# Kernel optimization log

Hardware: AMD Instinct MI355X
Metric: run time of the kernel (lower is better)

## Reference

```python
import jax, jax.numpy as jnp
import numpy as np

QMIN, QMAX = -128.0, 127.0  # int8 range


def setup_inputs() -> dict:
    key = jax.random.key(0)
    k1, k2, k3, k4 = jax.random.split(key, 4)
    B, S, K, O = 8, 2048, 4096, 4096
    x = jax.random.normal(k1, (B, S, K), dtype=jnp.float32)
    weight = jax.random.normal(k2, (O, K), dtype=jnp.float32)
    bias = jax.random.normal(k3, (O,), dtype=jnp.float32)
    # per-tensor activation qparams (static, from calibration observer)
    act_scale = jnp.ones((1,), dtype=jnp.float32) * 0.05
    act_zp = jnp.zeros((1,), dtype=jnp.int32)
    # per-output-row weight qparams (block_size = (1, in_features))
    weight_scale = jax.random.uniform(k4, (O, 1), dtype=jnp.float32,
                                      minval=0.005, maxval=0.02)
    weight_zp = jnp.zeros((O, 1), dtype=jnp.int32)
    return {"x": x, "weight": weight, "bias": bias,
            "act_scale": act_scale, "weight_scale": weight_scale,
            "act_zp": act_zp, "weight_zp": weight_zp}


def _quant_dequant(v, scale, zp):
    # affine quantize to int8 grid, then dequantize (simulated int8 math)
    q = jnp.clip(jnp.round(v / scale) + zp.astype(v.dtype), QMIN, QMAX)
    return (q - zp.astype(v.dtype)) * scale


def reference(x, weight, bias, act_scale, weight_scale, act_zp, weight_zp):
    # static per-tensor activation quantization
    dqx = _quant_dequant(x, act_scale, act_zp)          # [B, S, K]
    # per-row weight quantization
    dqw = _quant_dequant(weight, weight_scale, weight_zp)  # [O, K]
    # F.linear: x @ W^T + b
    return jnp.einsum('bsk,ok->bso', dqx, dqw) + bias
```

## Files before the change

kernel.cpp:

```cpp
#include <hip/hip_runtime.h>
#include <cstdint>
#include <cstddef>

typedef __attribute__((ext_vector_type(4)))  int   i32x4;
typedef __attribute__((ext_vector_type(16))) int   i32x16;
typedef __attribute__((ext_vector_type(4)))  float f32x4;

#define M_DIM 16384
#define N_DIM 4096
#define K_DIM 4096
#define NT    (K_DIM / 128)

#define BARRIER() asm volatile("s_barrier" ::: "memory")

__global__ __launch_bounds__(256) void quant_x_kernel(
    const float* __restrict__ x,
    const float* __restrict__ act_scale,
    const int*   __restrict__ act_zp,
    signed char* __restrict__ xq)
{
    int idx = blockIdx.x * 256 + threadIdx.x;
    float s   = act_scale[0];
    float zpf = (float)act_zp[0];
    const f32x4* xp = (const f32x4*)(x + (size_t)idx * 16);
    union { signed char c[16]; i32x4 v; } u;
#pragma unroll
    for (int j = 0; j < 4; ++j) {
        f32x4 v = xp[j];
#pragma unroll
        for (int e = 0; e < 4; ++e) {
            float q = rintf(v[e] / s) + zpf;
            q = fminf(fmaxf(q, -128.f), 127.f);
            u.c[j * 4 + e] = (signed char)(int)(q - zpf);
        }
    }
    *(i32x4*)(xq + (size_t)idx * 16) = u.v;
}

__global__ __launch_bounds__(256) void quant_w_kernel(
    const float* __restrict__ w,
    const float* __restrict__ wscale,
    const int*   __restrict__ wzp,
    signed char* __restrict__ wq)
{
    int idx = blockIdx.x * 256 + threadIdx.x;
    int row = idx >> 8;
    float s   = wscale[row];
    float zpf = (float)wzp[row];
    const f32x4* wp = (const f32x4*)(w + (size_t)idx * 16);
    union { signed char c[16]; i32x4 v; } u;
#pragma unroll
    for (int j = 0; j < 4; ++j) {
        f32x4 v = wp[j];
#pragma unroll
        for (int e = 0; e < 4; ++e) {
            float q = rintf(v[e] / s) + zpf;
            q = fminf(fmaxf(q, -128.f), 127.f);
            u.c[j * 4 + e] = (signed char)(int)(q - zpf);
        }
    }
    *(i32x4*)(wq + (size_t)idx * 16) = u.v;
}

__global__ __launch_bounds__(512, 2) void gemm_i8_256(
    const signed char* __restrict__ Aq,
    const signed char* __restrict__ Bq,
    const float* __restrict__ bias,
    const float* __restrict__ act_scale,
    const float* __restrict__ wscale,
    float* __restrict__ out)
{
    __shared__ signed char lds[65536];

    const int nbn = N_DIM / 256;
    const int nwg = (M_DIM / 256) * nbn;
    int bid = blockIdx.x;
    int wg  = (bid & 7) * (nwg >> 3) + (bid >> 3);
    int bm  = wg / nbn;
    int bn  = wg % nbn;

    int tid  = threadIdx.x;
    int wave = tid >> 6;
    int lane = tid & 63;
    int wm_i = wave >> 2;
    int wn_i = wave & 3;

    const signed char* Ag = Aq + (size_t)bm * 256 * K_DIM;
    const signed char* Bg = Bq + (size_t)bn * 256 * K_DIM;

    size_t soff = (size_t)(tid >> 1) * K_DIM + (((tid & 1) ^ ((tid >> 3) & 1)) * 16);

    int xbit  = (((lane >> 5) ^ ((lane >> 2) & 1)) << 4);
    int abase = wm_i * 4096 + (lane & 31) * 32 + xbit;
    int bbase = 32768 + wn_i * 2048 + (lane & 31) * 32 + xbit;

#define STAGE_AB(tile, s) do {                                                       \
    __builtin_amdgcn_global_load_lds(                                                \
        (const __attribute__((address_space(1))) void*)                              \
            (Ag + (size_t)(tile) * 128 + (s) * 32 + soff),                           \
        (__attribute__((address_space(3))) void*)(lds + (s) * 8192 + wave * 1024),   \
        16, 0, 0);                                                                   \
    __builtin_amdgcn_global_load_lds(                                                \
        (const __attribute__((address_space(1))) void*)                              \
            (Bg + (size_t)(tile) * 128 + (s) * 32 + soff),                           \
        (__attribute__((address_space(3))) void*)(lds + 32768 + (s) * 8192           \
                                                  + wave * 1024),                    \
        16, 0, 0);                                                                   \
} while (0)

#define READ_SET(AF, BF, s) do {                                                     \
    _Pragma("unroll")                                                                \
    for (int mf = 0; mf < 4; ++mf)                                                   \
        AF[mf] = *(const i32x4*)(lds + (s) * 8192 + abase + mf * 1024);              \
    _Pragma("unroll")                                                                \
    for (int nf = 0; nf < 2; ++nf)                                                   \
        BF[nf] = *(const i32x4*)(lds + (s) * 8192 + bbase + nf * 1024);              \
} while (0)

#define MFMA_SET(AF, BF) do {                                                        \
    _Pragma("unroll")                                                                \
    for (int mf = 0; mf < 4; ++mf)                                                   \
        _Pragma("unroll")                                                            \
        for (int nf = 0; nf < 2; ++nf)                                               \
            acc[mf][nf] = __builtin_amdgcn_mfma_i32_32x32x32_i8(                     \
                AF[mf], BF[nf], acc[mf][nf], 0, 0, 0);                               \
} while (0)

    i32x16 acc[4][2] = {};
    i32x4 aE[4], bE[2], aO[4], bO[2];

    STAGE_AB(0, 0); STAGE_AB(0, 1); STAGE_AB(0, 2); STAGE_AB(0, 3);
    asm volatile("s_waitcnt vmcnt(0)" ::: "memory");
    BARRIER();
    READ_SET(aE, bE, 0);
    asm volatile("s_waitcnt lgkmcnt(0)" ::: "memory");
    BARRIER();

#define PHASE(t, s, CA, CB, NA, NB) do {                                             \
    if ((t) + 1 < NT) {                                                              \
        STAGE_AB((t) + 1, (s));                                                      \
        if ((s) == 3) READ_SET(NA, NB, 0);               \
    }                                                                                \
    if ((s) < 3) READ_SET(NA, NB, (s) + 1);                         \
    __builtin_amdgcn_s_setprio(1);                                                   \
    MFMA_SET(CA, CB);                                                                \
    __builtin_amdgcn_s_setprio(0);                                                   \
    asm volatile("s_waitcnt lgkmcnt(0)" ::: "memory");                               \
    if ((t) < NT - 1) {                                                              \
        asm volatile("s_waitcnt vmcnt(4)" ::: "memory");                             \
    } else if ((s) == 0) {                                                           \
        asm volatile("s_waitcnt vmcnt(2)" ::: "memory");                             \
    } else if ((s) == 1) {                                                           \
        asm volatile("s_waitcnt vmcnt(0)" ::: "memory");                             \
    }                                                                                \
    BARRIER();                                                                       \
} while (0)

    for (int t = 0; t < NT; ++t) {
        PHASE(t, 0, aE, bE, aO, bO);
        PHASE(t, 1, aO, bO, aE, bE);
        PHASE(t, 2, aE, bE, aO, bO);
        PHASE(t, 3, aO, bO, aE, bE);
    }
#undef PHASE
#undef MFMA_SET
#undef READ_SET
#undef STAGE_AB

    float sa = act_scale[0];
#pragma unroll
    for (int nf = 0; nf < 2; ++nf) {
        int o = bn * 256 + wn_i * 64 + nf * 32 + (lane & 31);
        float sw = sa * wscale[o];
        float bv = bias[o];
#pragma unroll
        for (int mf = 0; mf < 4; ++mf) {
            int rowb = bm * 256 + wm_i * 128 + mf * 32 + 4 * (lane >> 5);
#pragma unroll
            for (int r = 0; r < 16; ++r) {
                int grow = rowb + (r & 3) + 8 * (r >> 2);
                out[(size_t)grow * N_DIM + o] = (float)acc[mf][nf][r] * sw + bv;
            }
        }
    }
}

__global__ void fallback_kernel(
    const float* __restrict__ x, const float* __restrict__ w,
    const float* __restrict__ bias,
    const float* __restrict__ act_scale, const float* __restrict__ wscale,
    const int* __restrict__ act_zp, const int* __restrict__ wzp,
    float* __restrict__ out)
{
    size_t idx = (size_t)blockIdx.x * blockDim.x + threadIdx.x;
    if (idx >= (size_t)M_DIM * N_DIM) return;
    int m = (int)(idx >> 12);
    int o = (int)(idx & 4095);
    float sx = act_scale[0], zx = (float)act_zp[0];
    float sw = wscale[o],    zw = (float)wzp[o];
    float acc = 0.f;
    for (int k = 0; k < K_DIM; ++k) {
        float qx = fminf(fmaxf(rintf(x[(size_t)m * K_DIM + k] / sx) + zx, -128.f), 127.f) - zx;
        float qw = fminf(fmaxf(rintf(w[(size_t)o * K_DIM + k] / sw) + zw, -128.f), 127.f) - zw;
        acc += (qx * sx) * (qw * sw);
    }
    out[idx] = acc + bias[o];
}

extern "C" void kernel_launch(void* const* d_in, const int* in_sizes, int n_in,
                              void* d_out, int out_size, void* d_ws, size_t ws_size,
                              hipStream_t stream)
{
    const float* x    = (const float*)d_in[0];
    const float* w    = (const float*)d_in[1];
    const float* bias = (const float*)d_in[2];
    const float* asc  = (const float*)d_in[3];
    const float* wsc  = (const float*)d_in[4];
    const int*   azp  = (const int*)d_in[5];
    const int*   wzp  = (const int*)d_in[6];
    float* out = (float*)d_out;

    size_t xq_bytes = (size_t)M_DIM * K_DIM;
    size_t wq_bytes = (size_t)N_DIM * K_DIM;

    if (ws_size < xq_bytes + wq_bytes) {
        int total = M_DIM * N_DIM;
        fallback_kernel<<<(total + 255) / 256, 256, 0, stream>>>(
            x, w, bias, asc, wsc, azp, wzp, out);
        return;
    }

    signed char* xq = (signed char*)d_ws;
    signed char* wq = (signed char*)d_ws + xq_bytes;

    quant_x_kernel<<<(M_DIM * (K_DIM / 16)) / 256, 256, 0, stream>>>(x, asc, azp, xq);
    quant_w_kernel<<<(N_DIM * (K_DIM / 16)) / 256, 256, 0, stream>>>(w, wsc, wzp, wq);
    gemm_i8_256<<<(M_DIM / 256) * (N_DIM / 256), 512, 0, stream>>>(
        xq, wq, bias, asc, wsc, out);
}
```

Baseline: 449.0 us.

## Double-buffer full K-tiles in LDS with new swizzled layout

Replaces the four-stage ring of 32-wide K sub-slices with two full 128-wide K-tile buffers (128 KB LDS). Each iteration prefetches the next whole tile while running four MFMA groups on the current one. There is one barrier per tile instead of one per sub-stage. Staging and read addressing change to a new XOR-swizzled layout meant to avoid LDS bank conflicts. LDS use doubles, which drops the occupancy from 2 workgroups per CU to 1. The full vmcnt(0) wait at the end of each tile may expose global-load latency.

```diff
diff --git a/kernel.cpp b/kernel.cpp
--- a/kernel.cpp
+++ b/kernel.cpp
@@ -70,7 +70,7 @@
     const float* __restrict__ wscale,
     float* __restrict__ out)
 {
-    __shared__ signed char lds[65536];
+    __shared__ signed char lds[131072];
 
     const int nbn = N_DIM / 256;
     const int nwg = (M_DIM / 256) * nbn;
@@ -88,33 +88,42 @@
     const signed char* Ag = Aq + (size_t)bm * 256 * K_DIM;
     const signed char* Bg = Bq + (size_t)bn * 256 * K_DIM;
 
-    size_t soff = (size_t)(tid >> 1) * K_DIM + (((tid & 1) ^ ((tid >> 3) & 1)) * 16);
-
-    int xbit  = (((lane >> 5) ^ ((lane >> 2) & 1)) << 4);
-    int abase = wm_i * 4096 + (lane & 31) * 32 + xbit;
-    int bbase = 32768 + wn_i * 2048 + (lane & 31) * 32 + xbit;
-
-#define STAGE_AB(tile, s) do {                                                       \
-    __builtin_amdgcn_global_load_lds(                                                \
-        (const __attribute__((address_space(1))) void*)                              \
-            (Ag + (size_t)(tile) * 128 + (s) * 32 + soff),                           \
-        (__attribute__((address_space(3))) void*)(lds + (s) * 8192 + wave * 1024),   \
-        16, 0, 0);                                                                   \
-    __builtin_amdgcn_global_load_lds(                                                \
-        (const __attribute__((address_space(1))) void*)                              \
-            (Bg + (size_t)(tile) * 128 + (s) * 32 + soff),                           \
-        (__attribute__((address_space(3))) void*)(lds + 32768 + (s) * 8192           \
-                                                  + wave * 1024),                    \
-        16, 0, 0);                                                                   \
+    int srow = ((lane ^ (lane >> 3)) & 3) * 8 + ((lane >> 3) & 7);
+    int sg   = ((lane >> 2) ^ (lane >> 5)) & 1;
+    size_t rowK = (size_t)srow * K_DIM + sg * 16;
+    const signed char* Asrc = Ag + (size_t)(wave * 32) * K_DIM + rowK;
+    const signed char* Bsrc = Bg + (size_t)(wave * 32) * K_DIM + rowK;
+
+    int laneoff = (lane & 7) * 128
+                + (((lane & 7) ^ ((lane >> 5) << 2) ^ ((lane >> 3) & 3)) * 16);
+    int abase = wm_i * 16384;
+    int bbase = 32768 + wn_i * 8192;
+
+#define STAGE_TILE(tile, dbase) do {                                                 \
+    _Pragma("unroll")                                                                \
+    for (int ks = 0; ks < 4; ++ks) {                                                 \
+        __builtin_amdgcn_global_load_lds(                                            \
+            (const __attribute__((address_space(1))) void*)                          \
+                (Asrc + (size_t)(tile) * 128 + ks * 32),                             \
+            (__attribute__((address_space(3))) void*)                                \
+                (lds + (dbase) + (wave * 4 + ks) * 1024), 16, 0, 0);                 \
+        __builtin_amdgcn_global_load_lds(                                            \
+            (const __attribute__((address_space(1))) void*)                          \
+                (Bsrc + (size_t)(tile) * 128 + ks * 32),                             \
+            (__attribute__((address_space(3))) void*)                                \
+                (lds + (dbase) + 32768 + (wave * 4 + ks) * 1024), 16, 0, 0);         \
+    }                                                                                \
 } while (0)
 
-#define READ_SET(AF, BF, s) do {                                                     \
+#define READ_SET(AF, BF, cbase, ks) do {                                             \
     _Pragma("unroll")                                                                \
     for (int mf = 0; mf < 4; ++mf)                                                   \
-        AF[mf] = *(const i32x4*)(lds + (s) * 8192 + abase + mf * 1024);              \
+        AF[mf] = *(const i32x4*)(lds + (cbase) + abase + mf * 4096                   \
+                                 + (ks) * 1024 + laneoff);                           \
     _Pragma("unroll")                                                                \
     for (int nf = 0; nf < 2; ++nf)                                                   \
-        BF[nf] = *(const i32x4*)(lds + (s) * 8192 + bbase + nf * 1024);              \
+        BF[nf] = *(const i32x4*)(lds + (cbase) + bbase + nf * 4096                   \
+                                 + (ks) * 1024 + laneoff);                           \
 } while (0)
 
 #define MFMA_SET(AF, BF) do {                                                        \
@@ -129,43 +138,43 @@
     i32x16 acc[4][2] = {};
     i32x4 aE[4], bE[2], aO[4], bO[2];
 
-    STAGE_AB(0, 0); STAGE_AB(0, 1); STAGE_AB(0, 2); STAGE_AB(0, 3);
+    STAGE_TILE(0, 0);
     asm volatile("s_waitcnt vmcnt(0)" ::: "memory");
     BARRIER();
-    READ_SET(aE, bE, 0);
-    asm volatile("s_waitcnt lgkmcnt(0)" ::: "memory");
-    BARRIER();
-
-#define PHASE(t, s, CA, CB, NA, NB) do {                                             \
-    if ((t) + 1 < NT) {                                                              \
-        STAGE_AB((t) + 1, (s));                                                      \
-        if ((s) == 3) READ_SET(NA, NB, 0);               \
-    }                                                                                \
-    if ((s) < 3) READ_SET(NA, NB, (s) + 1);                         \
-    __builtin_amdgcn_s_setprio(1);                                                   \
-    MFMA_SET(CA, CB);                                                                \
-    __builtin_amdgcn_s_setprio(0);                                                   \
-    asm volatile("s_waitcnt lgkmcnt(0)" ::: "memory");                               \
-    if ((t) < NT - 1) {                                                              \
-        asm volatile("s_waitcnt vmcnt(4)" ::: "memory");                             \
-    } else if ((s) == 0) {                                                           \
-        asm volatile("s_waitcnt vmcnt(2)" ::: "memory");                             \
-    } else if ((s) == 1) {                                                           \
-        asm volatile("s_waitcnt vmcnt(0)" ::: "memory");                             \
-    }                                                                                \
-    BARRIER();                                                                       \
-} while (0)
 
     for (int t = 0; t < NT; ++t) {
-        PHASE(t, 0, aE, bE, aO, bO);
-        PHASE(t, 1, aO, bO, aE, bE);
-        PHASE(t, 2, aE, bE, aO, bO);
-        PHASE(t, 3, aO, bO, aE, bE);
-    }
-#undef PHASE
+        const int cb = (t & 1) * 65536;
+        const int nb = cb ^ 65536;
+
+        if (t + 1 < NT) STAGE_TILE(t + 1, nb);
+
+        READ_SET(aE, bE, cb, 0);
+        READ_SET(aO, bO, cb, 1);
+        __builtin_amdgcn_s_setprio(1); MFMA_SET(aE, bE);
+        __builtin_amdgcn_s_setprio(0);
+        __builtin_amdgcn_sched_barrier(0);
+
+        READ_SET(aE, bE, cb, 2);
+        __builtin_amdgcn_s_setprio(1); MFMA_SET(aO, bO);
+        __builtin_amdgcn_s_setprio(0);
+        __builtin_amdgcn_sched_barrier(0);
+
+        READ_SET(aO, bO, cb, 3);
+        __builtin_amdgcn_s_setprio(1); MFMA_SET(aE, bE);
+        __builtin_amdgcn_s_setprio(0);
+        __builtin_amdgcn_sched_barrier(0);
+
+        __builtin_amdgcn_s_setprio(1); MFMA_SET(aO, bO);
+        __builtin_amdgcn_s_setprio(0);
+
+        if (t + 1 < NT) {
+            asm volatile("s_waitcnt lgkmcnt(0) vmcnt(0)" ::: "memory");
+            BARRIER();
+        }
+    }
 #undef MFMA_SET
 #undef READ_SET
-#undef STAGE_AB
+#undef STAGE_TILE
 
     float sa = act_scale[0];
 #pragma unroll
```

Result: slower. 470.1 us (+4.7%).
